# Kernel tuning notes

Hardware: AMD Instinct MI355X
Metric: run time of the kernel (lower is better)

Reference implementation:

```python
import jax, jax.numpy as jnp
import numpy as np

BS, N, N_HEAD, F_IN, F_OUT = 8, 1024, 8, 256, 64
NEG_SLOPE = 0.2


def setup_inputs() -> dict:
    key = jax.random.key(0)
    k_h, k_adj, k_w, k_src, k_dst = jax.random.split(key, 5)
    h = jax.random.normal(k_h, (BS, N, F_IN), dtype=jnp.float32)
    adj = jax.random.randint(k_adj, (BS, N, N), 0, 2) > 0  # bool adjacency
    # xavier_uniform-style params
    def xavier(k, shape, fan_in, fan_out):
        limit = float(np.sqrt(6.0 / (fan_in + fan_out)))
        return jax.random.uniform(k, shape, jnp.float32, -limit, limit)
    w = xavier(k_w, (N_HEAD, F_IN, F_OUT), F_IN, F_OUT)
    a_src = xavier(k_src, (N_HEAD, F_OUT, 1), F_OUT, 1)
    a_dst = xavier(k_dst, (N_HEAD, F_OUT, 1), F_OUT, 1)
    bias = jnp.zeros((F_OUT,), dtype=jnp.float32)
    return {"h": h, "adj": adj, "w": w, "a_src": a_src, "a_dst": a_dst, "bias": bias}


def reference(h, adj, w, a_src, a_dst, bias):
    # h: [bs, n, f_in], w: [n_head, f_in, f_out]
    h_prime = jnp.einsum('bnf,hfo->bhno', h, w)            # [bs, h, n, f_out]
    t = jnp.tanh(h_prime)
    attn_src = jnp.einsum('bhno,ho->bhn', t, a_src[..., 0])  # [bs, h, n]
    attn_dst = jnp.einsum('bhno,ho->bhn', t, a_dst[..., 0])  # [bs, h, n]
    attn = attn_src[:, :, :, None] + attn_dst[:, :, None, :]  # [bs, h, n, n]
    attn = jnp.where(attn >= 0, attn, NEG_SLOPE * attn)       # leaky_relu(0.2)
    n = adj.shape[-1]
    mask = ~(adj[:, None, :, :] | jnp.eye(n, dtype=bool))     # [bs, 1->h, n, n]
    attn = jnp.where(mask, -jnp.inf, attn)
    attn = jax.nn.softmax(attn, axis=-1)                      # diag always valid
    out = jnp.einsum('bhnm,bhmo->bhno', attn, h_prime)
    return out + bias
```

## Files before the change

kernel.cpp:

```cpp
#include <hip/hip_runtime.h>
#include <math.h>

#define BS 8
#define NPTS 1024
#define NH 8
#define FIN 256
#define FOUT 64

typedef __attribute__((ext_vector_type(8))) short s8v;
typedef __attribute__((ext_vector_type(8))) _Float16 h8v;
typedef __attribute__((ext_vector_type(2))) __fp16 fp16x2;
typedef __attribute__((ext_vector_type(4))) float f4v;
typedef unsigned long long u64;

__device__ __forceinline__ unsigned short f2bf(float f) {
  unsigned u = __float_as_uint(f);
  return (unsigned short)((u + 0x7fffu + ((u >> 16) & 1u)) >> 16);
}
__device__ __forceinline__ float bf2f(unsigned short s) {
  return __uint_as_float(((unsigned)s) << 16);
}
__device__ __forceinline__ float fast_tanh(float x) {
  float e = __expf(2.f * x);
  return 1.f - 2.f / (e + 1.f);
}
__device__ __forceinline__ float hw_exp2(float x) {
  float r;
  asm("v_exp_f32 %0, %1" : "=v"(r) : "v"(x));
  return r;
}

__device__ __forceinline__ void gl_lds16(const void* g, void* l) {
  __builtin_amdgcn_global_load_lds(
      (const __attribute__((address_space(1))) unsigned*)g,
      (__attribute__((address_space(3))) unsigned*)l, 16, 0, 0);
}

__global__ __launch_bounds__(256) void prep_kernel(
    const void* __restrict__ adjv, const float* __restrict__ w,
    const float* __restrict__ h,
    u64* __restrict__ abits,
    unsigned short* __restrict__ wT_hi, unsigned short* __restrict__ wT_lo,
    unsigned short* __restrict__ hs_hi, unsigned short* __restrict__ hs_lo)
{
  const int blk = blockIdx.x;
  const int t = threadIdx.x;
  if (blk < 2048) {
    __shared__ int badsh;
    if (t == 0) badsh = 0;
    __syncthreads();
    if (((const unsigned*)adjv)[t] > 1u) badsh = 1;
    __syncthreads();
    const int lane = t & 63;
    const int gw = blk * 4 + (t >> 6);
    const int b = gw >> 10, i = gw & 1023;
    const int m16 = lane & 15, g = lane >> 4;
    u64 words[4];
    if (badsh == 0) {
      const int4* row4 = (const int4*)((const int*)adjv + ((size_t)b * NPTS + i) * NPTS);
      int4 av[4];
      av[0] = row4[lane]; av[1] = row4[lane + 64];
      av[2] = row4[lane + 128]; av[3] = row4[lane + 192];
#pragma unroll
      for (int ci = 0; ci < 4; ++ci) {
        unsigned n = (unsigned)(av[ci].x != 0) | ((unsigned)(av[ci].y != 0) << 1) |
                     ((unsigned)(av[ci].z != 0) << 2) | ((unsigned)(av[ci].w != 0) << 3);
        unsigned d = (unsigned)(i - (ci * 256 + 4 * lane));
        if (d < 4u) n |= 1u << d;
        u64 val = (u64)n << (4 * m16);
#pragma unroll
        for (int msk = 1; msk <= 8; msk <<= 1)
          val |= (u64)__shfl_xor(val, msk, 64);
        words[ci] = val;
      }
    } else {
      const unsigned* rowB = (const unsigned*)((const unsigned char*)adjv + ((size_t)b * NPTS + i) * NPTS);
      unsigned av[4];
      av[0] = rowB[lane]; av[1] = rowB[lane + 64];
      av[2] = rowB[lane + 128]; av[3] = rowB[lane + 192];
#pragma unroll
      for (int ci = 0; ci < 4; ++ci) {
        unsigned v = av[ci];
        unsigned n = ((v & 0xffu) ? 1u : 0u) | (((v >> 8) & 0xffu) ? 2u : 0u) |
                     (((v >> 16) & 0xffu) ? 4u : 0u) | ((v >> 24) ? 8u : 0u);
        unsigned d = (unsigned)(i - (ci * 256 + 4 * lane));
        if (d < 4u) n |= 1u << d;
        u64 val = (u64)n << (4 * m16);
#pragma unroll
        for (int msk = 1; msk <= 8; msk <<= 1)
          val |= (u64)__shfl_xor(val, msk, 64);
        words[ci] = val;
      }
    }
    if (m16 == 0) {
#pragma unroll
      for (int ci = 0; ci < 4; ++ci)
        abits[((size_t)b * NPTS + i) * 16 + ci * 4 + g] = words[ci];
    }
  } else if (blk < 2112) {
    const int bb = blk - 2048;
    const int hh = bb >> 3, ks = bb & 7;
    const int o = t & 63, kq = t >> 6;
#pragma unroll
    for (int e = 0; e < 8; ++e) {
      int k = ks * 32 + kq * 8 + e;
      float v = w[((size_t)hh * FIN + k) * FOUT + o];
      unsigned short hi = f2bf(v);
      wT_hi[((size_t)hh * FOUT + o) * FIN + k] = hi;
      wT_lo[((size_t)hh * FOUT + o) * FIN + k] = f2bf(v - bf2f(hi));
    }
  } else {
    const size_t g = (size_t)(blk - 2112) * 256 + t;
    const float4* hp4 = (const float4*)h + g * 2;
    float4 v0 = hp4[0], v1 = hp4[1];
    float vv[8] = {v0.x, v0.y, v0.z, v0.w, v1.x, v1.y, v1.z, v1.w};
    unsigned short hb[8], lb[8];
#pragma unroll
    for (int e = 0; e < 8; ++e) {
      unsigned u = __float_as_uint(vv[e]);
      float r = vv[e] - __uint_as_float(u & 0xffff0000u);
      hb[e] = (unsigned short)(u >> 16);
      lb[e] = (unsigned short)(__float_as_uint(r) >> 16);
    }
    *(uint4*)(hs_hi + g * 8) = *(const uint4*)&hb[0];
    *(uint4*)(hs_lo + g * 8) = *(const uint4*)&lb[0];
  }
}

__global__ __launch_bounds__(256, 4) void proj_kernel(
    const unsigned short* __restrict__ hs_hi, const unsigned short* __restrict__ hs_lo,
    const unsigned short* __restrict__ wT_hi, const unsigned short* __restrict__ wT_lo,
    const float* __restrict__ a_src, const float* __restrict__ a_dst,
    unsigned short* __restrict__ hfrag,
    float* __restrict__ srcb, float* __restrict__ dstb)
{
  __shared__ unsigned short Bbuf[2][4096];
  __shared__ float tile[64][65];

  const int t = threadIdx.x;
  const int lane = t & 63;
  const int wv = t >> 6;
  const int blk = blockIdx.x;
  const int it = blk & 15;
  const int hh = (blk >> 4) & 7;
  const int b  = blk >> 7;
  const int i0 = it * 64;
  const int bh = b * NH + hh;
  const int l15 = lane & 15;
  const int g4  = lane >> 4;
  const int koff = g4 * 8;

  const int o_t  = t >> 2;
  const int gsrc = (t & 3) ^ ((o_t >> 1) & 3);
  const unsigned short* gB_hi = wT_hi + ((size_t)(hh * FOUT + o_t)) * FIN + gsrc * 8;
  const unsigned short* gB_lo = wT_lo + ((size_t)(hh * FOUT + o_t)) * FIN + gsrc * 8;

  const unsigned short* arow_hi = hs_hi + ((size_t)(b * NPTS + i0 + wv * 16 + l15)) * FIN + koff;
  const unsigned short* arow_lo = hs_lo + ((size_t)(b * NPTS + i0 + wv * 16 + l15)) * FIN + koff;

  const int sw = (l15 >> 1) & 3;
  int roff[4];
#pragma unroll
  for (int nt = 0; nt < 4; ++nt)
    roff[nt] = (nt * 16 + l15) * 32 + (g4 ^ sw) * 8;

  gl_lds16(gB_hi, &Bbuf[0][wv * 512]);
  gl_lds16(gB_lo, &Bbuf[0][2048 + wv * 512]);
  s8v Ah = *(const s8v*)(arow_hi);
  s8v Al = *(const s8v*)(arow_lo);

  f4v acc[4];
#pragma unroll
  for (int nt = 0; nt < 4; ++nt) acc[nt] = 0.0f;
  __syncthreads();

#pragma unroll
  for (int k0 = 0; k0 < 8; ++k0) {
    const int buf = k0 & 1;
    s8v Ah_n = Ah, Al_n = Al;
    if (k0 < 7) {
      gl_lds16(gB_hi + (k0 + 1) * 32, &Bbuf[buf ^ 1][wv * 512]);
      gl_lds16(gB_lo + (k0 + 1) * 32, &Bbuf[buf ^ 1][2048 + wv * 512]);
      Ah_n = *(const s8v*)(arow_hi + (k0 + 1) * 32);
      Al_n = *(const s8v*)(arow_lo + (k0 + 1) * 32);
    }
    const unsigned short* fb = &Bbuf[buf][0];
#pragma unroll
    for (int nt = 0; nt < 4; ++nt) {
      s8v Bh = *(const s8v*)(fb + roff[nt]);
      s8v Bl = *(const s8v*)(fb + 2048 + roff[nt]);
      acc[nt] = __builtin_amdgcn_mfma_f32_16x16x32_bf16(Ah, Bh, acc[nt], 0, 0, 0);
      acc[nt] = __builtin_amdgcn_mfma_f32_16x16x32_bf16(Al, Bh, acc[nt], 0, 0, 0);
      acc[nt] = __builtin_amdgcn_mfma_f32_16x16x32_bf16(Ah, Bl, acc[nt], 0, 0, 0);
    }
    Ah = Ah_n; Al = Al_n;
    __syncthreads();
  }

  float a_s[4], a_d[4];
#pragma unroll
  for (int nt = 0; nt < 4; ++nt) {
    a_s[nt] = a_src[hh * FOUT + nt * 16 + l15];
    a_d[nt] = a_dst[hh * FOUT + nt * 16 + l15];
  }
#pragma unroll
  for (int qq = 0; qq < 4; ++qq) {
    float ps = 0.f, pd = 0.f;
#pragma unroll
    for (int nt = 0; nt < 4; ++nt) {
      float tv = fast_tanh(acc[nt][qq]);
      ps = fmaf(tv, a_s[nt], ps);
      pd = fmaf(tv, a_d[nt], pd);
    }
#pragma unroll
    for (int m = 8; m >= 1; m >>= 1) {
      ps += __shfl_xor(ps, m, 64);
      pd += __shfl_xor(pd, m, 64);
    }
    if (l15 == 0) {
      int row = i0 + wv * 16 + g4 * 4 + qq;
      srcb[(size_t)bh * NPTS + row] = ps;
      dstb[(size_t)bh * NPTS + row] = pd;
    }
  }

#pragma unroll
  for (int nt = 0; nt < 4; ++nt)
#pragma unroll
    for (int qq = 0; qq < 4; ++qq)
      tile[wv * 16 + g4 * 4 + qq][nt * 16 + l15] = acc[nt][qq];
  __syncthreads();

  const int cbase = t >> 6;
#pragma unroll
  for (int ci = 0; ci < 2; ++ci) {
    int cc = cbase + ci * 4;
    int ks = cc >> 2, nt2 = cc & 3;
    int jb = ks * 32 + ((lane >> 4) * 8);
    int ob = nt2 * 16 + l15;
    h8v v;
#pragma unroll
    for (int e = 0; e < 8; ++e) v[e] = (_Float16)tile[jb + e][ob];
    *(h8v*)(hfrag + (((size_t)(bh * 16 + it) * 8 + cc) * 64 + lane) * 8) = v;
  }
}

__global__ __launch_bounds__(256, 4) void attn_kernel(
    const u64* __restrict__ abits,
    const unsigned short* __restrict__ hfrag,
    const float* __restrict__ srcb, const float* __restrict__ dstb,
    const float* __restrict__ bias, float* __restrict__ out)
{
  __shared__ float dsh[NPTS];
  __shared__ float wred[4];
  __shared__ uint2 mlut[16];
  __shared__ unsigned short frag[2][8192];

  const int t = threadIdx.x;
  const int lane = t & 63;
  const int wv = t >> 6;
  const int blk = blockIdx.x;
  const int it = blk & 15;
  const int hh = (blk >> 4) & 7;
  const int b  = blk >> 7;
  const int i0 = it * 64;
  const int bh = b * NH + hh;
  const int l15 = lane & 15;
  const int koff = (lane >> 4) * 8;
  const int rowA = i0 + wv * 16 + l15;

  const uint4* fgb = (const uint4*)hfrag + (size_t)bh * 16 * 512;
  const uint4* abrow4 = (const uint4*)(abits + ((size_t)b * NPTS + rowA) * 16);

  uint4 s0 = fgb[t];
  uint4 s1 = fgb[t + 256];
  uint4 s2 = fgb[t + 512];
  uint4 s3 = fgb[t + 768];
  uint4 ab_cur = abrow4[0];
  const float src_r = srcb[(size_t)bh * NPTS + rowA];
  float4 dv = ((const float4*)(dstb + (size_t)bh * NPTS))[t];

  if (t < 16) {
    unsigned m = t;
    mlut[t] = make_uint2(
        ((m & 1u) ? 0xFFFFu : 0u) | (((m >> 1) & 1u) ? 0xFFFF0000u : 0u),
        (((m >> 2) & 1u) ? 0xFFFFu : 0u) | (((m >> 3) & 1u) ? 0xFFFF0000u : 0u));
  }

  const float L2E = 1.44269504f;
  float4 dsc;
  dsc.x = dv.x * L2E; dsc.y = dv.y * L2E; dsc.z = dv.z * L2E; dsc.w = dv.w * L2E;
  ((float4*)dsh)[t] = dsc;
  float lm = fmaxf(fmaxf(dv.x, dv.y), fmaxf(dv.z, dv.w));
#pragma unroll
  for (int m = 32; m >= 1; m >>= 1) lm = fmaxf(lm, __shfl_xor(lm, m, 64));
  if (lane == 0) wred[wv] = lm;
  __syncthreads();
  const float M = fmaxf(fmaxf(wred[0], wred[1]), fmaxf(wred[2], wred[3]));
  const float xm = src_r + M;
  const float m_row = fmaxf(xm, 0.2f * xm);
  const float c1s = (src_r - m_row) * L2E;
  const float c2s = (0.2f * src_r - m_row) * L2E;

  {
    uint4* dstf = (uint4*)&frag[0][0];
    dstf[t] = s0; dstf[t + 256] = s1; dstf[t + 512] = s2; dstf[t + 768] = s3;
  }
  __syncthreads();

  h8v ones;
#pragma unroll
  for (int e = 0; e < 8; ++e) ones[e] = (_Float16)1.0f;

  f4v acc[4], acc_l;
#pragma unroll
  for (int nt = 0; nt < 4; ++nt) acc[nt] = 0.0f;
  acc_l = 0.0f;

#pragma unroll 2
  for (int jt = 0; jt < 8; ++jt) {
    const int buf = jt & 1;
    uint4 n0, n1, n2, n3, ab_nxt;
    if (jt < 7) {
      const uint4* fgn = fgb + (size_t)(jt + 1) * 1024;
      n0 = fgn[t]; n1 = fgn[t + 256]; n2 = fgn[t + 512]; n3 = fgn[t + 768];
      ab_nxt = abrow4[jt + 1];
    }
    __builtin_amdgcn_sched_barrier(0);

    h8v pa[2][2];
    const unsigned wbits[4] = {ab_cur.x, ab_cur.y, ab_cur.z, ab_cur.w};
#pragma unroll
    for (int s = 0; s < 2; ++s)
#pragma unroll
      for (int ks = 0; ks < 2; ++ks) {
        const int jb = jt * 128 + s * 64 + ks * 32 + koff;
        float4 d0 = *(const float4*)&dsh[jb];
        float4 d1 = *(const float4*)&dsh[jb + 4];
        float dl[8] = {d0.x, d0.y, d0.z, d0.w, d1.x, d1.y, d1.z, d1.w};
        const unsigned wq = wbits[s * 2 + ks] >> koff;
        float pe[8];
#pragma unroll
        for (int e = 0; e < 8; ++e) {
          float arg = fmaxf(c1s + dl[e], fmaf(0.2f, dl[e], c2s));
          pe[e] = hw_exp2(arg);
        }
        union { fp16x2 q[4]; unsigned u[4]; h8v v; } uu;
        uu.q[0] = __builtin_amdgcn_cvt_pkrtz(pe[0], pe[1]);
        uu.q[1] = __builtin_amdgcn_cvt_pkrtz(pe[2], pe[3]);
        uu.q[2] = __builtin_amdgcn_cvt_pkrtz(pe[4], pe[5]);
        uu.q[3] = __builtin_amdgcn_cvt_pkrtz(pe[6], pe[7]);
        uint2 m0 = mlut[wq & 15], m1 = mlut[(wq >> 4) & 15];
        uu.u[0] &= m0.x; uu.u[1] &= m0.y; uu.u[2] &= m1.x; uu.u[3] &= m1.y;
        pa[s][ks] = uu.v;
      }

    __builtin_amdgcn_s_setprio(1);
#pragma unroll
    for (int s = 0; s < 2; ++s) {
#pragma unroll
      for (int ks = 0; ks < 2; ++ks) {
#pragma unroll
        for (int nt = 0; nt < 4; ++nt) {
          h8v B = *(const h8v*)&frag[buf][(((s * 8 + ks * 4 + nt) * 64) + lane) * 8];
          acc[nt] = __builtin_amdgcn_mfma_f32_16x16x32_f16(pa[s][ks], B, acc[nt], 0, 0, 0);
        }
        acc_l = __builtin_amdgcn_mfma_f32_16x16x32_f16(pa[s][ks], ones, acc_l, 0, 0, 0);
      }
    }
    __builtin_amdgcn_s_setprio(0);

    if (jt < 7) {
      uint4* dstf = (uint4*)&frag[buf ^ 1][0];
      dstf[t] = n0; dstf[t + 256] = n1; dstf[t + 512] = n2; dstf[t + 768] = n3;
      ab_cur = ab_nxt;
    }
    __syncthreads();
  }

  float bias4[4];
#pragma unroll
  for (int nt = 0; nt < 4; ++nt) bias4[nt] = bias[nt * 16 + l15];

#pragma unroll
  for (int qq = 0; qq < 4; ++qq) {
    float linv = 1.0f / acc_l[qq];
    int rowq = i0 + wv * 16 + (lane >> 4) * 4 + qq;
    size_t ob = ((size_t)bh * NPTS + rowq) * FOUT;
#pragma unroll
    for (int nt = 0; nt < 4; ++nt)
      out[ob + nt * 16 + l15] = acc[nt][qq] * linv + bias4[nt];
  }
}

extern "C" void kernel_launch(void* const* d_in, const int* in_sizes, int n_in,
                              void* d_out, int out_size, void* d_ws, size_t ws_size,
                              hipStream_t stream)
{
  const float* h     = (const float*)d_in[0];
  const void*  adj   = d_in[1];
  const float* w     = (const float*)d_in[2];
  const float* a_src = (const float*)d_in[3];
  const float* a_dst = (const float*)d_in[4];
  const float* bias  = (const float*)d_in[5];
  float* out = (float*)d_out;

  char* p = (char*)d_ws;
  float* srcb = (float*)p;                      p += (size_t)BS * NH * NPTS * 4;
  float* dstb = (float*)p;                      p += (size_t)BS * NH * NPTS * 4;
  unsigned short* wT_hi = (unsigned short*)p;   p += (size_t)NH * FOUT * FIN * 2;
  unsigned short* wT_lo = (unsigned short*)p;   p += (size_t)NH * FOUT * FIN * 2;
  u64* abits = (u64*)p;                         p += (size_t)BS * NPTS * 16 * 8;
  unsigned short* hs_hi = (unsigned short*)p;   p += (size_t)BS * NPTS * FIN * 2;
  unsigned short* hs_lo = (unsigned short*)p;   p += (size_t)BS * NPTS * FIN * 2;
  unsigned short* hfrag = (unsigned short*)p;

  prep_kernel<<<dim3(3136), dim3(256), 0, stream>>>(
      adj, w, h, abits, wT_hi, wT_lo, hs_hi, hs_lo);
  proj_kernel<<<dim3(1024), dim3(256), 0, stream>>>(
      hs_hi, hs_lo, wT_hi, wT_lo, a_src, a_dst, hfrag, srcb, dstb);
  attn_kernel<<<dim3(1024), dim3(256), 0, stream>>>(
      abits, hfrag, srcb, dstb, bias, out);
}
```

Measured before the change: 52.15 us.

## Triple-buffer projection K-loop with one barrier per step and union LDS

The projection kernel's K loop moves from double to triple buffering. Two stages are prefetched ahead, and explicit vmcnt waits plus a single s_barrier per iteration replace the two __syncthreads. The B buffers and the output tile now share LDS through a union, so shared memory use stays roughly flat. The aim is to hide global-to-LDS load latency and cut barrier count. The cost is hand-counted vmcnt values that must match the number of outstanding loads exactly.

```diff
diff --git a/kernel.cpp b/kernel.cpp
--- a/kernel.cpp
+++ b/kernel.cpp
@@ -127,6 +127,11 @@
   }
 }
 
+union ProjSmem {
+  unsigned short Bbuf[3][4096];
+  float tile[64][65];
+};
+
 __global__ __launch_bounds__(256, 4) void proj_kernel(
     const unsigned short* __restrict__ hs_hi, const unsigned short* __restrict__ hs_lo,
     const unsigned short* __restrict__ wT_hi, const unsigned short* __restrict__ wT_lo,
@@ -134,8 +139,7 @@
     unsigned short* __restrict__ hfrag,
     float* __restrict__ srcb, float* __restrict__ dstb)
 {
-  __shared__ unsigned short Bbuf[2][4096];
-  __shared__ float tile[64][65];
+  __shared__ ProjSmem sm;
 
   const int t = threadIdx.x;
   const int lane = t & 63;
@@ -164,38 +168,48 @@
   for (int nt = 0; nt < 4; ++nt)
     roff[nt] = (nt * 16 + l15) * 32 + (g4 ^ sw) * 8;
 
-  gl_lds16(gB_hi, &Bbuf[0][wv * 512]);
-  gl_lds16(gB_lo, &Bbuf[0][2048 + wv * 512]);
-  s8v Ah = *(const s8v*)(arow_hi);
-  s8v Al = *(const s8v*)(arow_lo);
+  s8v Ah[3], Al[3];
+  gl_lds16(gB_hi, &sm.Bbuf[0][wv * 512]);
+  gl_lds16(gB_lo, &sm.Bbuf[0][2048 + wv * 512]);
+  Ah[0] = *(const s8v*)(arow_hi);
+  Al[0] = *(const s8v*)(arow_lo);
+  gl_lds16(gB_hi + 32, &sm.Bbuf[1][wv * 512]);
+  gl_lds16(gB_lo + 32, &sm.Bbuf[1][2048 + wv * 512]);
+  Ah[1] = *(const s8v*)(arow_hi + 32);
+  Al[1] = *(const s8v*)(arow_lo + 32);
 
   f4v acc[4];
 #pragma unroll
   for (int nt = 0; nt < 4; ++nt) acc[nt] = 0.0f;
-  __syncthreads();
 
 #pragma unroll
   for (int k0 = 0; k0 < 8; ++k0) {
-    const int buf = k0 & 1;
-    s8v Ah_n = Ah, Al_n = Al;
-    if (k0 < 7) {
-      gl_lds16(gB_hi + (k0 + 1) * 32, &Bbuf[buf ^ 1][wv * 512]);
-      gl_lds16(gB_lo + (k0 + 1) * 32, &Bbuf[buf ^ 1][2048 + wv * 512]);
-      Ah_n = *(const s8v*)(arow_hi + (k0 + 1) * 32);
-      Al_n = *(const s8v*)(arow_lo + (k0 + 1) * 32);
-    }
-    const unsigned short* fb = &Bbuf[buf][0];
+    if (k0 == 7) asm volatile("s_waitcnt vmcnt(0)" ::: "memory");
+    else         asm volatile("s_waitcnt vmcnt(4)" ::: "memory");
+    __builtin_amdgcn_sched_barrier(0);
+    __builtin_amdgcn_s_barrier();
+    __builtin_amdgcn_sched_barrier(0);
+
+    if (k0 < 6) {
+      const int nb = (k0 + 2) % 3;
+      gl_lds16(gB_hi + (k0 + 2) * 32, &sm.Bbuf[nb][wv * 512]);
+      gl_lds16(gB_lo + (k0 + 2) * 32, &sm.Bbuf[nb][2048 + wv * 512]);
+      Ah[nb] = *(const s8v*)(arow_hi + (k0 + 2) * 32);
+      Al[nb] = *(const s8v*)(arow_lo + (k0 + 2) * 32);
+    }
+
+    const int cb = k0 % 3;
+    const unsigned short* fb = &sm.Bbuf[cb][0];
 #pragma unroll
     for (int nt = 0; nt < 4; ++nt) {
       s8v Bh = *(const s8v*)(fb + roff[nt]);
       s8v Bl = *(const s8v*)(fb + 2048 + roff[nt]);
-      acc[nt] = __builtin_amdgcn_mfma_f32_16x16x32_bf16(Ah, Bh, acc[nt], 0, 0, 0);
-      acc[nt] = __builtin_amdgcn_mfma_f32_16x16x32_bf16(Al, Bh, acc[nt], 0, 0, 0);
-      acc[nt] = __builtin_amdgcn_mfma_f32_16x16x32_bf16(Ah, Bl, acc[nt], 0, 0, 0);
-    }
-    Ah = Ah_n; Al = Al_n;
-    __syncthreads();
-  }
+      acc[nt] = __builtin_amdgcn_mfma_f32_16x16x32_bf16(Ah[cb], Bh, acc[nt], 0, 0, 0);
+      acc[nt] = __builtin_amdgcn_mfma_f32_16x16x32_bf16(Al[cb], Bh, acc[nt], 0, 0, 0);
+      acc[nt] = __builtin_amdgcn_mfma_f32_16x16x32_bf16(Ah[cb], Bl, acc[nt], 0, 0, 0);
+    }
+  }
+  __syncthreads();
 
   float a_s[4], a_d[4];
 #pragma unroll
@@ -228,7 +242,7 @@
   for (int nt = 0; nt < 4; ++nt)
 #pragma unroll
     for (int qq = 0; qq < 4; ++qq)
-      tile[wv * 16 + g4 * 4 + qq][nt * 16 + l15] = acc[nt][qq];
+      sm.tile[wv * 16 + g4 * 4 + qq][nt * 16 + l15] = acc[nt][qq];
   __syncthreads();
 
   const int cbase = t >> 6;
@@ -240,7 +254,7 @@
     int ob = nt2 * 16 + l15;
     h8v v;
 #pragma unroll
-    for (int e = 0; e < 8; ++e) v[e] = (_Float16)tile[jb + e][ob];
+    for (int e = 0; e < 8; ++e) v[e] = (_Float16)sm.tile[jb + e][ob];
     *(h8v*)(hfrag + (((size_t)(bh * 16 + it) * 8 + cc) * 64 + lane) * 8) = v;
   }
 }
```

After: 52.06 us. Within noise of the previous version (-0.2%).
